# Performance work log

Hardware: AMD Instinct MI355X
Metric: run time of the kernel (lower is better)

The kernel has to match this reference:

```python
import jax, jax.numpy as jnp
import numpy as np

MIN_NORM = 1e-5
PROJ_EPS = 4e-3  # geoopt poincare ball boundary eps


def expmap0(u, c):
    # exponential map at origin of the Poincare ball: tanh(sqrt(c)||u||) * u / (sqrt(c)||u||)
    sqrt_c = jnp.sqrt(c)
    u_norm = jnp.maximum(jnp.linalg.norm(u, axis=-1, keepdims=True), MIN_NORM)
    return jnp.tanh(sqrt_c * u_norm) * u / (sqrt_c * u_norm)


def project(x, c):
    # clip points to stay strictly inside the ball of radius (1-eps)/sqrt(c)
    norm = jnp.maximum(jnp.linalg.norm(x, axis=-1, keepdims=True), MIN_NORM)
    maxnorm = (1.0 - PROJ_EPS) / jnp.sqrt(c)
    return jnp.where(norm > maxnorm, x / norm * maxnorm, x)


def setup_inputs() -> dict:
    key = jax.random.key(0)
    k1, k2, k3 = jax.random.split(key, 3)
    n, m, d = 4096, 4096, 1024
    query = jax.random.normal(k1, (n, d), dtype=jnp.float32)
    context = jax.random.normal(k2, (m, d), dtype=jnp.float32)
    W = jax.random.normal(k3, (d, d), dtype=jnp.float32) / np.sqrt(d)  # linear_in weight
    c = jnp.ones((1,), dtype=jnp.float32)  # curvature parameter
    return {"query": query, "context": context, "W": W, "c": c}


def reference(query, context, W, c):
    n, d = query.shape
    q = project(expmap0(query, c), c)
    ctx = project(expmap0(context, c), c)
    q = q @ W.T                      # linear_in (no bias), [n, d]
    scores = q @ ctx.T               # [n, m]
    attn = jax.nn.softmax(scores / d, axis=1)
    attn = project(expmap0(attn, c), c)
    return attn
```

## Files before the change

kernel.cpp:

```cpp
#include <hip/hip_runtime.h>
#include <cstdint>


typedef unsigned short ushort_t;
typedef __bf16 bf16x8 __attribute__((ext_vector_type(8)));
typedef float f32x4 __attribute__((ext_vector_type(4)));

__device__ __forceinline__ unsigned short f32_to_bf16(float f) {
  unsigned int u = __float_as_uint(f);
  u = (u + 0x7fffu + ((u >> 16) & 1u)) >> 16;
  return (unsigned short)u;
}

__device__ __forceinline__ void async_copy16(const void* g, void* s) {
  __builtin_amdgcn_global_load_lds(
      (const __attribute__((address_space(1))) void*)g,
      (__attribute__((address_space(3))) void*)s, 16, 0, 0);
}

__global__ void prep_q(const float* __restrict__ q, const float* __restrict__ W,
                       ushort_t* __restrict__ qn, ushort_t* __restrict__ Wb,
                       const float* __restrict__ cptr, int n) {
  const int b = blockIdx.x;
  const int tid = threadIdx.x;

  if (b >= n) {
    int i = (b - n) * 256 + tid;
    float4 v = reinterpret_cast<const float4*>(W)[i];
    reinterpret_cast<ushort4*>(Wb)[i] =
        make_ushort4(f32_to_bf16(v.x), f32_to_bf16(v.y), f32_to_bf16(v.z), f32_to_bf16(v.w));
    return;
  }

  const int lane = tid & 63, w = tid >> 6;
  __shared__ float red[4];
  const float* x = q + (size_t)b * 1024;
  ushort_t* out = qn + (size_t)b * 1024;

  float4 v = reinterpret_cast<const float4*>(x)[tid];
  float ss = v.x * v.x + v.y * v.y + v.z * v.z + v.w * v.w;
#pragma unroll
  for (int o = 32; o; o >>= 1) ss += __shfl_down(ss, o, 64);
  if (lane == 0) red[w] = ss;
  __syncthreads();
  ss = red[0] + red[1] + red[2] + red[3];

  const float c = *cptr;
  const float sqrtc = sqrtf(c);
  const float norm = fmaxf(sqrtf(ss), 1e-5f);
  const float t = tanhf(sqrtc * norm) / (sqrtc * norm);
  const float en = fmaxf(t * norm, 1e-5f);
  const float maxn = (1.0f - 4e-3f) / sqrtc;
  const float s = t * (en > maxn ? maxn / en : 1.0f);

  reinterpret_cast<ushort4*>(out)[tid] =
      make_ushort4(f32_to_bf16(v.x * s), f32_to_bf16(v.y * s),
                   f32_to_bf16(v.z * s), f32_to_bf16(v.w * s));
}

__global__ void qw_ctx(const ushort_t* __restrict__ A,
                       const ushort_t* __restrict__ B,
                       ushort_t* __restrict__ Cb,
                       const float* __restrict__ ctx, ushort_t* __restrict__ cn,
                       const float* __restrict__ cptr, int K, int N, int nGemm) {
  __shared__ __align__(16) ushort_t As[128 * 32];
  __shared__ __align__(16) ushort_t Bs[64 * 32];

  const int tid = threadIdx.x;

  if (blockIdx.x >= nGemm) {
    const int r = blockIdx.x - nGemm;
    const int lane = tid & 63, wv = tid >> 6;
    float* red = reinterpret_cast<float*>(As);
    const float* x = ctx + (size_t)r * 1024;
    ushort_t* out = cn + (size_t)r * 1024;

    float4 v = reinterpret_cast<const float4*>(x)[tid];
    float ss = v.x * v.x + v.y * v.y + v.z * v.z + v.w * v.w;
#pragma unroll
    for (int o = 32; o; o >>= 1) ss += __shfl_down(ss, o, 64);
    if (lane == 0) red[wv] = ss;
    __syncthreads();
    ss = red[0] + red[1] + red[2] + red[3];

    const float c = *cptr;
    const float sqrtc = sqrtf(c);
    const float norm = fmaxf(sqrtf(ss), 1e-5f);
    const float t = tanhf(sqrtc * norm) / (sqrtc * norm);
    const float en = fmaxf(t * norm, 1e-5f);
    const float maxn = (1.0f - 4e-3f) / sqrtc;
    const float s = t * (en > maxn ? maxn / en : 1.0f);

    reinterpret_cast<ushort4*>(out)[tid] =
        make_ushort4(f32_to_bf16(v.x * s), f32_to_bf16(v.y * s),
                     f32_to_bf16(v.z * s), f32_to_bf16(v.w * s));
    return;
  }

  const int gx = blockIdx.x & 31;
  const int gy = blockIdx.x >> 5;
  const int w = tid >> 6;
  const int lane = tid & 63;
  const int lane15 = lane & 15;
  const int quad = lane >> 4;
  const int wr = w >> 1, wc = w & 1;

  const size_t rowBase = (size_t)gx * 128;
  const size_t colBase = (size_t)gy * 64;

  const int srow = lane >> 2;
  const int scolE = (lane & 3) * 8;
  const ushort_t* Ag = A + (rowBase + (size_t)(w * 32 + srow)) * K + scolE;
  const ushort_t* Bg = B + (colBase + (size_t)(w * 16 + srow)) * K + scolE;
  ushort_t* AsD = &As[w * 1024];
  ushort_t* BsD = &Bs[w * 512];

  f32x4 acc[4][2];
#pragma unroll
  for (int i = 0; i < 4; ++i)
#pragma unroll
    for (int j = 0; j < 2; ++j) acc[i][j] = f32x4{0.f, 0.f, 0.f, 0.f};

  for (int k0 = 0; k0 < K; k0 += 32) {
    async_copy16(Ag + k0, AsD);
    async_copy16(Ag + (size_t)16 * K + k0, AsD + 512);
    async_copy16(Bg + k0, BsD);
    __syncthreads();

    bf16x8 af[4], bv[2];
#pragma unroll
    for (int i = 0; i < 4; ++i)
      af[i] = *reinterpret_cast<const bf16x8*>(&As[(wr * 64 + i * 16 + lane15) * 32 + quad * 8]);
#pragma unroll
    for (int j = 0; j < 2; ++j)
      bv[j] = *reinterpret_cast<const bf16x8*>(&Bs[(wc * 32 + j * 16 + lane15) * 32 + quad * 8]);
#pragma unroll
    for (int i = 0; i < 4; ++i)
#pragma unroll
      for (int j = 0; j < 2; ++j)
        acc[i][j] = __builtin_amdgcn_mfma_f32_16x16x32_bf16(af[i], bv[j], acc[i][j], 0, 0, 0);
    __syncthreads();
  }

#pragma unroll
  for (int i = 0; i < 4; ++i)
#pragma unroll
    for (int j = 0; j < 2; ++j)
#pragma unroll
      for (int r = 0; r < 4; ++r) {
        size_t row = rowBase + (size_t)(wr * 64 + i * 16 + quad * 4 + r);
        size_t col = colBase + (size_t)(wc * 32 + j * 16 + lane15);
        Cb[row * N + col] = f32_to_bf16(acc[i][j][r]);
      }
}


#define LDF(base, off) \
  (*reinterpret_cast<const bf16x8*>(reinterpret_cast<const char*>(base) + (off)))

#define SUBTILE(BUF, DOSTAGE, K0S)                                                        \
  do {                                                                                    \
    const ushort_t* As_ = &As[BUF][0];                                                    \
    const ushort_t* Bs_ = &Bs[BUF][0];                                                    \
    bf16x8 a0[4], b0[4], a1[4], c0[4], c1[4], b1[4];                                      \
    _Pragma("unroll") for (int mi = 0; mi < 4; ++mi) a0[mi] = LDF(As_, aO0 + mi * 2048);  \
    _Pragma("unroll") for (int ni = 0; ni < 4; ++ni) b0[ni] = LDF(Bs_, bO0 + ni * 2048);  \
    __builtin_amdgcn_s_setprio(1);                                                        \
    _Pragma("unroll") for (int mi = 0; mi < 4; ++mi)                                      \
      _Pragma("unroll") for (int ni = 0; ni < 4; ++ni)                                    \
        acc[mi][ni] = __builtin_amdgcn_mfma_f32_16x16x32_bf16(a0[mi], b0[ni], acc[mi][ni], 0, 0, 0); \
    __builtin_amdgcn_s_setprio(0);                                                        \
    _Pragma("unroll") for (int mi = 0; mi < 4; ++mi) a1[mi] = LDF(As_, aO0 + (4 + mi) * 2048); \
    _Pragma("unroll") for (int mi = 0; mi < 4; ++mi) c0[mi] = LDF(As_, aO1 + mi * 2048);  \
    _Pragma("unroll") for (int mi = 0; mi < 4; ++mi) c1[mi] = LDF(As_, aO1 + (4 + mi) * 2048); \
    _Pragma("unroll") for (int ni = 0; ni < 4; ++ni) b1[ni] = LDF(Bs_, bO1 + ni * 2048);  \
    __builtin_amdgcn_s_setprio(1);                                                        \
    _Pragma("unroll") for (int mi = 0; mi < 4; ++mi)                                      \
      _Pragma("unroll") for (int ni = 0; ni < 4; ++ni)                                    \
        acc[4 + mi][ni] = __builtin_amdgcn_mfma_f32_16x16x32_bf16(a1[mi], b0[ni], acc[4 + mi][ni], 0, 0, 0); \
    __builtin_amdgcn_s_setprio(0);                                                        \
    asm volatile("s_waitcnt lgkmcnt(0)" ::: "memory");      \
    __builtin_amdgcn_sched_barrier(0);                                                    \
    __builtin_amdgcn_s_barrier();                          \
    if (DOSTAGE) {                      \
      async_copy16(Ag + (size_t)(K0S), &As[BUF][w * 512]);                                \
      async_copy16(Ag + (size_t)64 * K + (K0S), &As[BUF][4096 + w * 512]);                \
      async_copy16(Ag + (size_t)128 * K + (K0S), &As[BUF][8192 + w * 512]);               \
      async_copy16(Ag + (size_t)192 * K + (K0S), &As[BUF][12288 + w * 512]);              \
    }                                                                                     \
    __builtin_amdgcn_s_setprio(1);                                                        \
    _Pragma("unroll") for (int mi = 0; mi < 4; ++mi)                                      \
      _Pragma("unroll") for (int ni = 0; ni < 4; ++ni)                                    \
        acc[mi][ni] = __builtin_amdgcn_mfma_f32_16x16x32_bf16(c0[mi], b1[ni], acc[mi][ni], 0, 0, 0); \
    __builtin_amdgcn_s_setprio(0);                                                        \
    if (DOSTAGE) {                      \
      async_copy16(Bg + (size_t)(K0S), &Bs[BUF][w * 512]);                                \
      async_copy16(Bg + (size_t)64 * K + (K0S), &Bs[BUF][4096 + w * 512]);                \
      async_copy16(Bg + (size_t)128 * K + (K0S), &Bs[BUF][8192 + w * 512]);               \
      async_copy16(Bg + (size_t)192 * K + (K0S), &Bs[BUF][12288 + w * 512]);              \
    }                                                                                     \
    __builtin_amdgcn_s_setprio(1);                                                        \
    _Pragma("unroll") for (int mi = 0; mi < 4; ++mi)                                      \
      _Pragma("unroll") for (int ni = 0; ni < 4; ++ni)                                    \
        acc[4 + mi][ni] = __builtin_amdgcn_mfma_f32_16x16x32_bf16(c1[mi], b1[ni], acc[4 + mi][ni], 0, 0, 0); \
    __builtin_amdgcn_s_setprio(0);                                                        \
  } while (0)

__global__ __launch_bounds__(512) void gemm_sc(const ushort_t* __restrict__ A,
                                               const ushort_t* __restrict__ B,
                                               ushort_t* __restrict__ Sb, int K, int N) {
  __shared__ __align__(16) ushort_t As[2][16384];
  __shared__ __align__(16) ushort_t Bs[2][16384];

  const int tid = threadIdx.x;
  const int w = tid >> 6;
  const int lane = tid & 63;
  const int l15 = lane & 15;
  const int quad = lane >> 4;
  const int wm = w >> 2;
  const int wn = w & 3;

  const size_t rowBase = (size_t)blockIdx.x * 256;
  const size_t colBase = (size_t)blockIdx.y * 256;

  const int colsw = (((lane & 7) ^ ((lane >> 3) & 7)) * 8);
  const ushort_t* Ag = A + (rowBase + (size_t)(w * 8 + (lane >> 3))) * K + colsw;
  const ushort_t* Bg = B + (colBase + (size_t)(w * 8 + (lane >> 3))) * K + colsw;

  const int axor = (l15 & 7) << 4;
  const int aO0 = (((wm * 128 + l15) * 128) + 0 * 64 + quad * 16) ^ axor;
  const int aO1 = (((wm * 128 + l15) * 128) + 1 * 64 + quad * 16) ^ axor;
  const int bO0 = (((wn * 64 + l15) * 128) + 0 * 64 + quad * 16) ^ axor;
  const int bO1 = (((wn * 64 + l15) * 128) + 1 * 64 + quad * 16) ^ axor;

  f32x4 acc[8][4];
#pragma unroll
  for (int mi = 0; mi < 8; ++mi)
#pragma unroll
    for (int ni = 0; ni < 4; ++ni) acc[mi][ni] = f32x4{0.f, 0.f, 0.f, 0.f};

#pragma unroll
  for (int hk = 0; hk < 4; ++hk)
    async_copy16(Ag + (size_t)(hk * 64) * K, &As[0][hk * 4096 + w * 512]);
#pragma unroll
  for (int hk = 0; hk < 4; ++hk)
    async_copy16(Bg + (size_t)(hk * 64) * K, &Bs[0][hk * 4096 + w * 512]);
#pragma unroll
  for (int hk = 0; hk < 4; ++hk)
    async_copy16(Ag + (size_t)(hk * 64) * K + 64, &As[1][hk * 4096 + w * 512]);
#pragma unroll
  for (int hk = 0; hk < 4; ++hk)
    async_copy16(Bg + (size_t)(hk * 64) * K + 64, &Bs[1][hk * 4096 + w * 512]);
  asm volatile("s_waitcnt vmcnt(8)" ::: "memory");
  __builtin_amdgcn_s_barrier();

  for (int i = 0; i < 8; ++i) {
    const bool st = (i < 7);
    const int k0s = i * 128 + 128;
    SUBTILE(0, st, k0s);
    if (st) { asm volatile("s_waitcnt vmcnt(8)" ::: "memory"); }
    else    { asm volatile("s_waitcnt vmcnt(0)" ::: "memory"); }
    __builtin_amdgcn_s_barrier();
    SUBTILE(1, st, k0s + 64);
    if (st) {
      asm volatile("s_waitcnt vmcnt(8)" ::: "memory");
      __builtin_amdgcn_s_barrier();
    }
  }

#pragma unroll
  for (int mi = 0; mi < 8; ++mi)
#pragma unroll
    for (int ni = 0; ni < 4; ++ni)
#pragma unroll
      for (int r = 0; r < 4; ++r) {
        size_t row = rowBase + (size_t)(wm * 128 + mi * 16 + quad * 4 + r);
        size_t col = colBase + (size_t)(wn * 64 + ni * 16 + l15);
        Sb[row * N + col] = f32_to_bf16(acc[mi][ni][r]);
      }
}

__global__ void softmax_hyp(const ushort_t* __restrict__ S, float* __restrict__ out,
                            const float* __restrict__ cptr, float invd) {
  const int tid = threadIdx.x;
  const int lane = tid & 63, w = tid >> 6;
  __shared__ float redS[4], redQ[4];
  const ushort_t* rp = S + (size_t)blockIdx.x * 4096;
  float* op = out + (size_t)blockIdx.x * 4096;

  float e[16];
  float sum = 0.f, sq = 0.f;
#pragma unroll
  for (int i = 0; i < 2; ++i) {
    uint4 u = reinterpret_cast<const uint4*>(rp)[i * 256 + tid];
    unsigned int uw[4] = {u.x, u.y, u.z, u.w};
#pragma unroll
    for (int k = 0; k < 4; ++k) {
      float lo = __uint_as_float(uw[k] << 16);
      float hi = __uint_as_float(uw[k] & 0xffff0000u);
      float elo = __expf(lo * invd);
      float ehi = __expf(hi * invd);
      e[i * 8 + k * 2] = elo;
      e[i * 8 + k * 2 + 1] = ehi;
      sum += elo + ehi;
      sq += elo * elo + ehi * ehi;
    }
  }
#pragma unroll
  for (int o = 32; o; o >>= 1) {
    sum += __shfl_down(sum, o, 64);
    sq += __shfl_down(sq, o, 64);
  }
  if (lane == 0) { redS[w] = sum; redQ[w] = sq; }
  __syncthreads();
  sum = redS[0] + redS[1] + redS[2] + redS[3];
  sq = redQ[0] + redQ[1] + redQ[2] + redQ[3];

  const float c = *cptr;
  const float sqrtc = sqrtf(c);
  const float anorm = sqrtf(sq) / sum;
  const float an = fmaxf(anorm, 1e-5f);
  const float t = tanhf(sqrtc * an) / (sqrtc * an);
  const float pn = fmaxf(t * anorm, 1e-5f);
  const float maxn = (1.0f - 4e-3f) / sqrtc;
  const float g = t * (pn > maxn ? maxn / pn : 1.0f) / sum;

#pragma unroll
  for (int i = 0; i < 2; ++i)
#pragma unroll
    for (int k = 0; k < 2; ++k) {
      float4 o = make_float4(e[i * 8 + k * 4] * g, e[i * 8 + k * 4 + 1] * g,
                             e[i * 8 + k * 4 + 2] * g, e[i * 8 + k * 4 + 3] * g);
      reinterpret_cast<float4*>(op)[(i * 256 + tid) * 2 + k] = o;
    }
}

extern "C" void kernel_launch(void* const* d_in, const int* in_sizes, int n_in,
                              void* d_out, int out_size, void* d_ws, size_t ws_size,
                              hipStream_t stream) {
  const float* query = (const float*)d_in[0];
  const float* context = (const float*)d_in[1];
  const float* W = (const float*)d_in[2];
  const float* cptr = (const float*)d_in[3];

  const int d = 1024;
  const int n = in_sizes[0] / d;
  const int m = in_sizes[1] / d;

  ushort_t* cn = (ushort_t*)d_ws;
  ushort_t* qw = cn + (size_t)m * d;
  ushort_t* qn = qw + (size_t)n * d;
  ushort_t* Wb = qn + (size_t)n * d;
  ushort_t* scoresB = qn;
  float* attn = (float*)d_out;

  const int nGemm = (n / 128) * (d / 64);

  prep_q<<<n + d * d / 1024, 256, 0, stream>>>(query, W, qn, Wb, cptr, n);
  qw_ctx<<<nGemm + m, 256, 0, stream>>>(qn, Wb, qw, context, cn, cptr, d, d, nGemm);
  gemm_sc<<<dim3(n / 256, m / 256), 512, 0, stream>>>(qw, cn, scoresB, d, m);
  softmax_hyp<<<n, 256, 0, stream>>>(scoresB, attn, cptr, 1.0f / (float)d);
}
```

Before: 165.6 us.

## Switch score GEMM to FP8 with scaled 32x32x64 MFMA

The projected query and normalized context operands are now stored as FP8 instead of BF16, and the score GEMM is rewritten around the MFMA scale 32x32x64 f8f6f4 instruction with a new LDS layout, swizzle and fragment loads. The aim is to halve operand traffic and use higher-throughput FP8 matrix cores for the largest GEMM. The cost is lower precision in the scores, though dividing scores by d before the softmax likely limits the damage. It also changes the epilogue mapping to match 32x32 accumulator tiles.

```diff
diff --git a/kernel.cpp b/kernel.cpp
--- a/kernel.cpp
+++ b/kernel.cpp
@@ -5,11 +5,19 @@
 typedef unsigned short ushort_t;
 typedef __bf16 bf16x8 __attribute__((ext_vector_type(8)));
 typedef float f32x4 __attribute__((ext_vector_type(4)));
+typedef float f32x16 __attribute__((ext_vector_type(16)));
+typedef int i32x4 __attribute__((ext_vector_type(4)));
+typedef int i32x8 __attribute__((ext_vector_type(8)));
 
 __device__ __forceinline__ unsigned short f32_to_bf16(float f) {
   unsigned int u = __float_as_uint(f);
   u = (u + 0x7fffu + ((u >> 16) & 1u)) >> 16;
   return (unsigned short)u;
+}
+
+__device__ __forceinline__ unsigned char f32_to_fp8(float f) {
+  int p = __builtin_amdgcn_cvt_pk_fp8_f32(f, f, 0, false);
+  return (unsigned char)(p & 0xFF);
 }
 
 __device__ __forceinline__ void async_copy16(const void* g, void* s) {
@@ -60,8 +68,8 @@
 
 __global__ void qw_ctx(const ushort_t* __restrict__ A,
                        const ushort_t* __restrict__ B,
-                       ushort_t* __restrict__ Cb,
-                       const float* __restrict__ ctx, ushort_t* __restrict__ cn,
+                       unsigned char* __restrict__ Cb,
+                       const float* __restrict__ ctx, unsigned char* __restrict__ cn,
                        const float* __restrict__ cptr, int K, int N, int nGemm) {
   __shared__ __align__(16) ushort_t As[128 * 32];
   __shared__ __align__(16) ushort_t Bs[64 * 32];
@@ -73,7 +81,7 @@
     const int lane = tid & 63, wv = tid >> 6;
     float* red = reinterpret_cast<float*>(As);
     const float* x = ctx + (size_t)r * 1024;
-    ushort_t* out = cn + (size_t)r * 1024;
+    unsigned char* out = cn + (size_t)r * 1024;
 
     float4 v = reinterpret_cast<const float4*>(x)[tid];
     float ss = v.x * v.x + v.y * v.y + v.z * v.z + v.w * v.w;
@@ -91,9 +99,9 @@
     const float maxn = (1.0f - 4e-3f) / sqrtc;
     const float s = t * (en > maxn ? maxn / en : 1.0f);
 
-    reinterpret_cast<ushort4*>(out)[tid] =
-        make_ushort4(f32_to_bf16(v.x * s), f32_to_bf16(v.y * s),
-                     f32_to_bf16(v.z * s), f32_to_bf16(v.w * s));
+    int lo = __builtin_amdgcn_cvt_pk_fp8_f32(v.x * s, v.y * s, 0, false);
+    int pk = __builtin_amdgcn_cvt_pk_fp8_f32(v.z * s, v.w * s, lo, true);
+    reinterpret_cast<int*>(out)[tid] = pk;
     return;
   }
 
@@ -150,132 +158,127 @@
       for (int r = 0; r < 4; ++r) {
         size_t row = rowBase + (size_t)(wr * 64 + i * 16 + quad * 4 + r);
         size_t col = colBase + (size_t)(wc * 32 + j * 16 + lane15);
-        Cb[row * N + col] = f32_to_bf16(acc[i][j][r]);
+        Cb[row * N + col] = f32_to_fp8(acc[i][j][r]);
       }
 }
 
 
-#define LDF(base, off) \
-  (*reinterpret_cast<const bf16x8*>(reinterpret_cast<const char*>(base) + (off)))
-
-#define SUBTILE(BUF, DOSTAGE, K0S)                                                        \
-  do {                                                                                    \
-    const ushort_t* As_ = &As[BUF][0];                                                    \
-    const ushort_t* Bs_ = &Bs[BUF][0];                                                    \
-    bf16x8 a0[4], b0[4], a1[4], c0[4], c1[4], b1[4];                                      \
-    _Pragma("unroll") for (int mi = 0; mi < 4; ++mi) a0[mi] = LDF(As_, aO0 + mi * 2048);  \
-    _Pragma("unroll") for (int ni = 0; ni < 4; ++ni) b0[ni] = LDF(Bs_, bO0 + ni * 2048);  \
-    __builtin_amdgcn_s_setprio(1);                                                        \
-    _Pragma("unroll") for (int mi = 0; mi < 4; ++mi)                                      \
-      _Pragma("unroll") for (int ni = 0; ni < 4; ++ni)                                    \
-        acc[mi][ni] = __builtin_amdgcn_mfma_f32_16x16x32_bf16(a0[mi], b0[ni], acc[mi][ni], 0, 0, 0); \
-    __builtin_amdgcn_s_setprio(0);                                                        \
-    _Pragma("unroll") for (int mi = 0; mi < 4; ++mi) a1[mi] = LDF(As_, aO0 + (4 + mi) * 2048); \
-    _Pragma("unroll") for (int mi = 0; mi < 4; ++mi) c0[mi] = LDF(As_, aO1 + mi * 2048);  \
-    _Pragma("unroll") for (int mi = 0; mi < 4; ++mi) c1[mi] = LDF(As_, aO1 + (4 + mi) * 2048); \
-    _Pragma("unroll") for (int ni = 0; ni < 4; ++ni) b1[ni] = LDF(Bs_, bO1 + ni * 2048);  \
-    __builtin_amdgcn_s_setprio(1);                                                        \
-    _Pragma("unroll") for (int mi = 0; mi < 4; ++mi)                                      \
-      _Pragma("unroll") for (int ni = 0; ni < 4; ++ni)                                    \
-        acc[4 + mi][ni] = __builtin_amdgcn_mfma_f32_16x16x32_bf16(a1[mi], b0[ni], acc[4 + mi][ni], 0, 0, 0); \
-    __builtin_amdgcn_s_setprio(0);                                                        \
-    asm volatile("s_waitcnt lgkmcnt(0)" ::: "memory");      \
-    __builtin_amdgcn_sched_barrier(0);                                                    \
-    __builtin_amdgcn_s_barrier();                          \
-    if (DOSTAGE) {                      \
-      async_copy16(Ag + (size_t)(K0S), &As[BUF][w * 512]);                                \
-      async_copy16(Ag + (size_t)64 * K + (K0S), &As[BUF][4096 + w * 512]);                \
-      async_copy16(Ag + (size_t)128 * K + (K0S), &As[BUF][8192 + w * 512]);               \
-      async_copy16(Ag + (size_t)192 * K + (K0S), &As[BUF][12288 + w * 512]);              \
-    }                                                                                     \
-    __builtin_amdgcn_s_setprio(1);                                                        \
-    _Pragma("unroll") for (int mi = 0; mi < 4; ++mi)                                      \
-      _Pragma("unroll") for (int ni = 0; ni < 4; ++ni)                                    \
-        acc[mi][ni] = __builtin_amdgcn_mfma_f32_16x16x32_bf16(c0[mi], b1[ni], acc[mi][ni], 0, 0, 0); \
-    __builtin_amdgcn_s_setprio(0);                                                        \
-    if (DOSTAGE) {                      \
-      async_copy16(Bg + (size_t)(K0S), &Bs[BUF][w * 512]);                                \
-      async_copy16(Bg + (size_t)64 * K + (K0S), &Bs[BUF][4096 + w * 512]);                \
-      async_copy16(Bg + (size_t)128 * K + (K0S), &Bs[BUF][8192 + w * 512]);               \
-      async_copy16(Bg + (size_t)192 * K + (K0S), &Bs[BUF][12288 + w * 512]);              \
-    }                                                                                     \
-    __builtin_amdgcn_s_setprio(1);                                                        \
-    _Pragma("unroll") for (int mi = 0; mi < 4; ++mi)                                      \
-      _Pragma("unroll") for (int ni = 0; ni < 4; ++ni)                                    \
-        acc[4 + mi][ni] = __builtin_amdgcn_mfma_f32_16x16x32_bf16(c1[mi], b1[ni], acc[4 + mi][ni], 0, 0, 0); \
-    __builtin_amdgcn_s_setprio(0);                                                        \
+#define MFMA8(a, b, c) \
+  __builtin_amdgcn_mfma_scale_f32_32x32x64_f8f6f4(a, b, c, 0, 0, 0, 0x7F7F7F7F, 0, 0x7F7F7F7F)
+
+__device__ __forceinline__ i32x8 ld_frag(const unsigned char* p, int off) {
+  i32x4 lo = *reinterpret_cast<const i32x4*>(p + off);
+  i32x4 hi = *reinterpret_cast<const i32x4*>(p + (off ^ 16));
+  return __builtin_shufflevector(lo, hi, 0, 1, 2, 3, 4, 5, 6, 7);
+}
+
+#define SUBTILE8(BUF, DOSTAGE, K0S)                                              \
+  do {                                                                           \
+    const unsigned char* As_ = &As[BUF][0];                                      \
+    const unsigned char* Bs_ = &Bs[BUF][0];                                      \
+    i32x8 af0 = ld_frag(As_, aO);                                                \
+    i32x8 af1 = ld_frag(As_, aO + 2048);                                         \
+    i32x8 bf0 = ld_frag(Bs_, bO);                                                \
+    i32x8 bf1 = ld_frag(Bs_, bO + 2048);                                         \
+    __builtin_amdgcn_s_setprio(1);                                               \
+    acc[0][0] = MFMA8(af0, bf0, acc[0][0]);                                      \
+    acc[0][1] = MFMA8(af0, bf1, acc[0][1]);                                      \
+    acc[1][0] = MFMA8(af1, bf0, acc[1][0]);                                      \
+    acc[1][1] = MFMA8(af1, bf1, acc[1][1]);                                      \
+    __builtin_amdgcn_s_setprio(0);                                               \
+    i32x8 af2 = ld_frag(As_, aO + 2 * 2048);                                     \
+    i32x8 af3 = ld_frag(As_, aO + 3 * 2048);                                     \
+    __builtin_amdgcn_s_setprio(1);                                               \
+    acc[2][0] = MFMA8(af2, bf0, acc[2][0]);                                      \
+    acc[2][1] = MFMA8(af2, bf1, acc[2][1]);                                      \
+    __builtin_amdgcn_s_setprio(0);                                               \
+    asm volatile("s_waitcnt lgkmcnt(0)" ::: "memory"); \
+    __builtin_amdgcn_sched_barrier(0);                                           \
+    __builtin_amdgcn_s_barrier();                         \
+    if (DOSTAGE) {                             \
+      async_copy16(Ag + (size_t)(K0S), &As[BUF][w * 1024]);                      \
+      async_copy16(Ag + (size_t)128 * K + (K0S), &As[BUF][8192 + w * 1024]);     \
+    }                                                                            \
+    __builtin_amdgcn_s_setprio(1);                                               \
+    acc[3][0] = MFMA8(af3, bf0, acc[3][0]);                                      \
+    __builtin_amdgcn_s_setprio(0);                                               \
+    if (DOSTAGE) {                             \
+      async_copy16(Bg + (size_t)(K0S), &Bs[BUF][w * 1024]);                      \
+      async_copy16(Bg + (size_t)128 * K + (K0S), &Bs[BUF][8192 + w * 1024]);     \
+    }                                                                            \
+    __builtin_amdgcn_s_setprio(1);                                               \
+    acc[3][1] = MFMA8(af3, bf1, acc[3][1]);                                      \
+    __builtin_amdgcn_s_setprio(0);                                               \
   } while (0)
 
-__global__ __launch_bounds__(512) void gemm_sc(const ushort_t* __restrict__ A,
-                                               const ushort_t* __restrict__ B,
+__global__ __launch_bounds__(512) void gemm_sc(const unsigned char* __restrict__ A,
+                                               const unsigned char* __restrict__ B,
                                                ushort_t* __restrict__ Sb, int K, int N) {
-  __shared__ __align__(16) ushort_t As[2][16384];
-  __shared__ __align__(16) ushort_t Bs[2][16384];
+  __shared__ __align__(16) unsigned char As[2][16384];
+  __shared__ __align__(16) unsigned char Bs[2][16384];
 
   const int tid = threadIdx.x;
   const int w = tid >> 6;
   const int lane = tid & 63;
-  const int l15 = lane & 15;
-  const int quad = lane >> 4;
+  const int l31 = lane & 31;
   const int wm = w >> 2;
   const int wn = w & 3;
 
   const size_t rowBase = (size_t)blockIdx.x * 256;
   const size_t colBase = (size_t)blockIdx.y * 256;
 
-  const int colsw = (((lane & 7) ^ ((lane >> 3) & 7)) * 8);
-  const ushort_t* Ag = A + (rowBase + (size_t)(w * 8 + (lane >> 3))) * K + colsw;
-  const ushort_t* Bg = B + (colBase + (size_t)(w * 8 + (lane >> 3))) * K + colsw;
-
-  const int axor = (l15 & 7) << 4;
-  const int aO0 = (((wm * 128 + l15) * 128) + 0 * 64 + quad * 16) ^ axor;
-  const int aO1 = (((wm * 128 + l15) * 128) + 1 * 64 + quad * 16) ^ axor;
-  const int bO0 = (((wn * 64 + l15) * 128) + 0 * 64 + quad * 16) ^ axor;
-  const int bO1 = (((wn * 64 + l15) * 128) + 1 * 64 + quad * 16) ^ axor;
-
-  f32x4 acc[8][4];
-#pragma unroll
-  for (int mi = 0; mi < 8; ++mi)
-#pragma unroll
-    for (int ni = 0; ni < 4; ++ni) acc[mi][ni] = f32x4{0.f, 0.f, 0.f, 0.f};
-
-#pragma unroll
-  for (int hk = 0; hk < 4; ++hk)
-    async_copy16(Ag + (size_t)(hk * 64) * K, &As[0][hk * 4096 + w * 512]);
-#pragma unroll
-  for (int hk = 0; hk < 4; ++hk)
-    async_copy16(Bg + (size_t)(hk * 64) * K, &Bs[0][hk * 4096 + w * 512]);
-#pragma unroll
-  for (int hk = 0; hk < 4; ++hk)
-    async_copy16(Ag + (size_t)(hk * 64) * K + 64, &As[1][hk * 4096 + w * 512]);
-#pragma unroll
-  for (int hk = 0; hk < 4; ++hk)
-    async_copy16(Bg + (size_t)(hk * 64) * K + 64, &Bs[1][hk * 4096 + w * 512]);
-  asm volatile("s_waitcnt vmcnt(8)" ::: "memory");
+  const int srcC = ((tid & 3) ^ ((tid >> 3) & 3)) * 16;
+  const unsigned char* Ag = A + (rowBase + (size_t)(tid >> 2)) * K + srcC;
+  const unsigned char* Bg = B + (colBase + (size_t)(tid >> 2)) * K + srcC;
+
+  const int x2 = (lane >> 1) & 3;
+  const int kc0 = (lane >> 5) * 2;
+  const int chunkOff = (kc0 ^ x2) * 16;
+  const int aO = (wm * 128 + l31) * 64 + chunkOff;
+  const int bO = (wn * 64 + l31) * 64 + chunkOff;
+
+  f32x16 acc[4][2];
+#pragma unroll
+  for (int mi = 0; mi < 4; ++mi)
+#pragma unroll
+    for (int ni = 0; ni < 2; ++ni)
+#pragma unroll
+      for (int r = 0; r < 16; ++r) acc[mi][ni][r] = 0.f;
+
+  async_copy16(Ag, &As[0][w * 1024]);
+  async_copy16(Ag + (size_t)128 * K, &As[0][8192 + w * 1024]);
+  async_copy16(Bg, &Bs[0][w * 1024]);
+  async_copy16(Bg + (size_t)128 * K, &Bs[0][8192 + w * 1024]);
+  async_copy16(Ag + 64, &As[1][w * 1024]);
+  async_copy16(Ag + (size_t)128 * K + 64, &As[1][8192 + w * 1024]);
+  async_copy16(Bg + 64, &Bs[1][w * 1024]);
+  async_copy16(Bg + (size_t)128 * K + 64, &Bs[1][8192 + w * 1024]);
+  asm volatile("s_waitcnt vmcnt(4)" ::: "memory");
   __builtin_amdgcn_s_barrier();
 
   for (int i = 0; i < 8; ++i) {
     const bool st = (i < 7);
     const int k0s = i * 128 + 128;
-    SUBTILE(0, st, k0s);
-    if (st) { asm volatile("s_waitcnt vmcnt(8)" ::: "memory"); }
+    SUBTILE8(0, st, k0s);
+    if (st) { asm volatile("s_waitcnt vmcnt(4)" ::: "memory"); }
     else    { asm volatile("s_waitcnt vmcnt(0)" ::: "memory"); }
     __builtin_amdgcn_s_barrier();
-    SUBTILE(1, st, k0s + 64);
+    SUBTILE8(1, st, k0s + 64);
     if (st) {
-      asm volatile("s_waitcnt vmcnt(8)" ::: "memory");
+      asm volatile("s_waitcnt vmcnt(4)" ::: "memory");
       __builtin_amdgcn_s_barrier();
     }
   }
 
-#pragma unroll
-  for (int mi = 0; mi < 8; ++mi)
-#pragma unroll
-    for (int ni = 0; ni < 4; ++ni)
-#pragma unroll
-      for (int r = 0; r < 4; ++r) {
-        size_t row = rowBase + (size_t)(wm * 128 + mi * 16 + quad * 4 + r);
-        size_t col = colBase + (size_t)(wn * 64 + ni * 16 + l15);
+  const int rq = lane >> 5;
+#pragma unroll
+  for (int mi = 0; mi < 4; ++mi)
+#pragma unroll
+    for (int ni = 0; ni < 2; ++ni)
+#pragma unroll
+      for (int r = 0; r < 16; ++r) {
+        size_t row = rowBase + (size_t)(wm * 128 + mi * 32 + (r & 3) + 8 * (r >> 2) + 4 * rq);
+        size_t col = colBase + (size_t)(wn * 64 + ni * 32 + l31);
         Sb[row * N + col] = f32_to_bf16(acc[mi][ni][r]);
       }
 }
@@ -347,9 +350,9 @@
   const int n = in_sizes[0] / d;
   const int m = in_sizes[1] / d;
 
-  ushort_t* cn = (ushort_t*)d_ws;
-  ushort_t* qw = cn + (size_t)m * d;
-  ushort_t* qn = qw + (size_t)n * d;
+  unsigned char* cn8 = (unsigned char*)d_ws;
+  unsigned char* qw8 = cn8 + (size_t)m * d;
+  ushort_t* qn = (ushort_t*)(qw8 + (size_t)n * d);
   ushort_t* Wb = qn + (size_t)n * d;
   ushort_t* scoresB = qn;
   float* attn = (float*)d_out;
@@ -357,7 +360,7 @@
   const int nGemm = (n / 128) * (d / 64);
 
   prep_q<<<n + d * d / 1024, 256, 0, stream>>>(query, W, qn, Wb, cptr, n);
-  qw_ctx<<<nGemm + m, 256, 0, stream>>>(qn, Wb, qw, context, cn, cptr, d, d, nGemm);
-  gemm_sc<<<dim3(n / 256, m / 256), 512, 0, stream>>>(qw, cn, scoresB, d, m);
+  qw_ctx<<<nGemm + m, 256, 0, stream>>>(qn, Wb, qw8, context, cn8, cptr, d, d, nGemm);
+  gemm_sc<<<dim3(n / 256, m / 256), 512, 0, stream>>>(qw8, cn8, scoresB, d, m);
   softmax_hyp<<<n, 256, 0, stream>>>(scoresB, attn, cptr, 1.0f / (float)d);
 }
```

Result: faster. 150.9 us (-8.8%).
